# Kernel tuning notes

Hardware: AMD Instinct MI355X
Metric: run time of the kernel (lower is better)

Reference implementation:

```python
import jax, jax.numpy as jnp
import numpy as np

B, T, S, H, E, V = 32, 32, 64, 512, 512, 32000
NEG = -1e9


def setup_inputs() -> dict:
    key = jax.random.key(0)
    ks = jax.random.split(key, 12)
    g = lambda i, shape: jax.random.normal(ks[i], shape, jnp.float32) * 0.05
    return {
        "tgt_batch": jax.random.randint(ks[0], (B, T), 0, V),
        "len_src_batch": jnp.maximum(jax.random.randint(ks[1], (B,), 0, S), 1),
        "enc_outputs": g(2, (S, B, H)),
        "h0": g(3, (1, B, H)),
        "c0": g(4, (1, B, H)),
        "emb": g(5, (V, E)),
        "W_ih": g(6, (4 * H, E + H)),
        "W_hh": g(7, (4 * H, H)),
        "b_ih": jnp.zeros((4 * H,), jnp.float32),
        "b_hh": jnp.zeros((4 * H,), jnp.float32),
        "W_a": g(8, (H, H)),
        "W_c": g(9, (H, 2 * H)),
        "b_c": jnp.zeros((H,), jnp.float32),
        "W_o": g(10, (V, H)),
        "b_o": jnp.zeros((V,), jnp.float32),
    }


def reference(tgt_batch, len_src_batch, enc_outputs, h0, c0, emb,
              W_ih, W_hh, b_ih, b_hh, W_a, W_c, b_c, W_o, b_o):
    Sv = enc_outputs.shape[0]
    # source padding mask [B,S]
    mask = jnp.arange(Sv)[None, :] < len_src_batch[:, None]
    enc_bsh = enc_outputs.transpose(1, 0, 2)                    # [B,S,H]
    # 'general' attention: score(h,e) = h^T W_a e ; precompute W_a @ e
    proj = jnp.einsum('kh,bsh->bsk', W_a, enc_bsh)              # [B,S,H]
    tgt = tgt_batch.T                                           # [T,B]

    def step(carry, w):
        h, c, ah = carry                                        # each [B,H]
        x = emb[w]                                              # [B,E]
        inp = jnp.concatenate([x, ah], axis=1)                  # [B,E+H]
        gates = inp @ W_ih.T + b_ih + h @ W_hh.T + b_hh         # [B,4H]
        i, f, g, o = jnp.split(gates, 4, axis=1)                # torch gate order
        i, f, o = jax.nn.sigmoid(i), jax.nn.sigmoid(f), jax.nn.sigmoid(o)
        c2 = f * c + i * jnp.tanh(g)
        h2 = o * jnp.tanh(c2)                                   # rnn_output
        scores = jnp.einsum('bk,bsk->bs', h2, proj)
        align = jax.nn.softmax(jnp.where(mask, scores, NEG), axis=1)
        ctx = jnp.einsum('bs,bsh->bh', align, enc_bsh)          # bmm context
        ah2 = jnp.tanh(jnp.concatenate([h2, ctx], axis=1) @ W_c.T + b_c)
        logp = jax.nn.log_softmax(ah2 @ W_o.T + b_o, axis=1)    # [B,V]
        return (h2, c2, ah2), logp

    init = (h0[0], c0[0], jnp.zeros_like(h0[0]))
    _, dec_outputs = jax.lax.scan(step, init, tgt[:-1])         # [T-1,B,V]
    dec_output_words = jnp.argmax(dec_outputs, axis=-1)         # [T-1,B]
    return dec_outputs, dec_output_words
```

## Files before the change

kernel.cpp:

```cpp
#include <hip/hip_runtime.h>
#include <cmath>

#define Bc 32
#define Tc 32
#define Sc 64
#define Hc 512
#define Ec 512
#define Vc 32000
#define NEGC (-1e9f)
#define BH (Bc * Hc)
#define Mtot ((Tc - 1) * Bc)

__device__ __forceinline__ float sigf(float x) { return 1.0f / (1.0f + expf(-x)); }

__device__ __forceinline__ float dot4(const float* a, const float* b) {
    float4 x = *(const float4*)a;
    float4 y = *(const float4*)b;
    return x.x * y.x + x.y * y.y + x.z * y.z + x.w * y.w;
}

__global__ __launch_bounds__(256) void k_init(const float* __restrict__ h0,
                                              const float* __restrict__ c0,
                                              float* __restrict__ h, float* __restrict__ c,
                                              float* __restrict__ ah0) {
    int i = blockIdx.x * 256 + threadIdx.x;
    if (i < BH) { h[i] = h0[i]; c[i] = c0[i]; ah0[i] = 0.0f; }
}

__global__ __launch_bounds__(256) void k_proj(const float* __restrict__ W_a,
                                              const float* __restrict__ enc,
                                              float* __restrict__ proj) {
    int k = blockIdx.x * 256 + threadIdx.x;
    int s0 = blockIdx.y * 8;
    int b = blockIdx.z;
    __shared__ float se[8][Hc];
    for (int i = threadIdx.x; i < 8 * Hc; i += 256) {
        int ss = i >> 9, hh = i & (Hc - 1);
        se[ss][hh] = enc[((size_t)(s0 + ss) * Bc + b) * Hc + hh];
    }
    __syncthreads();
    const float* wr = W_a + (size_t)k * Hc;
    float acc[8];
#pragma unroll
    for (int ss = 0; ss < 8; ++ss) acc[ss] = 0.0f;
    for (int h = 0; h < Hc; h += 4) {
        float4 w = *(const float4*)(wr + h);
#pragma unroll
        for (int ss = 0; ss < 8; ++ss) {
            acc[ss] = fmaf(w.x, se[ss][h + 0], acc[ss]);
            acc[ss] = fmaf(w.y, se[ss][h + 1], acc[ss]);
            acc[ss] = fmaf(w.z, se[ss][h + 2], acc[ss]);
            acc[ss] = fmaf(w.w, se[ss][h + 3], acc[ss]);
        }
    }
#pragma unroll
    for (int ss = 0; ss < 8; ++ss)
        proj[((size_t)b * Sc + s0 + ss) * Hc + k] = acc[ss];
}

__global__ __launch_bounds__(256) void k_step1(const int* __restrict__ tgt,
                                               const float* __restrict__ emb,
                                               const float* __restrict__ W_ih,
                                               const float* __restrict__ W_hh,
                                               const float* __restrict__ b_ih,
                                               const float* __restrict__ b_hh,
                                               const float* __restrict__ h_prev,
                                               const float* __restrict__ c_prev,
                                               const float* __restrict__ ah_prev,
                                               float* __restrict__ h_new,
                                               float* __restrict__ c_new, int t) {
    int tid = threadIdx.x;
    int b = tid & 31;
    int q = (tid >> 5) & 3;
    int hl = tid >> 7;
    int h = blockIdx.x * 2 + hl;
    int j = q * Hc + h;
    int w = tgt[b * Tc + t];
    const float* x = emb + (size_t)w * Ec;
    const float* wi = W_ih + (size_t)j * (Ec + Hc);
    const float* wh = W_hh + (size_t)j * Hc;
    const float* ap = ah_prev + b * Hc;
    const float* hp = h_prev + b * Hc;
    float a0 = 0.f, a1 = 0.f, a2 = 0.f, a3 = 0.f;
    for (int e = 0; e < Ec; e += 16) {
        a0 += dot4(x + e, wi + e);
        a1 += dot4(x + e + 4, wi + e + 4);
        a2 += dot4(x + e + 8, wi + e + 8);
        a3 += dot4(x + e + 12, wi + e + 12);
    }
    for (int k = 0; k < Hc; k += 16) {
        a0 += dot4(ap + k, wi + Ec + k);
        a1 += dot4(ap + k + 4, wi + Ec + k + 4);
        a2 += dot4(ap + k + 8, wi + Ec + k + 8);
        a3 += dot4(ap + k + 12, wi + Ec + k + 12);
    }
    for (int k = 0; k < Hc; k += 16) {
        a0 += dot4(hp + k, wh + k);
        a1 += dot4(hp + k + 4, wh + k + 4);
        a2 += dot4(hp + k + 8, wh + k + 8);
        a3 += dot4(hp + k + 12, wh + k + 12);
    }
    float acc = b_ih[j] + b_hh[j] + ((a0 + a1) + (a2 + a3));

    __shared__ float sg[2][4][32];
    sg[hl][q][b] = acc;
    __syncthreads();
    if (q == 0) {
        float iv = sigf(sg[hl][0][b]);
        float fv = sigf(sg[hl][1][b]);
        float gv = tanhf(sg[hl][2][b]);
        float ov = sigf(sg[hl][3][b]);
        int idx = b * Hc + h;
        float c2 = fv * c_prev[idx] + iv * gv;
        float h2 = ov * tanhf(c2);
        c_new[idx] = c2;
        h_new[idx] = h2;
    }
}

__global__ __launch_bounds__(256) void k_score(const float* __restrict__ proj,
                                               const float* __restrict__ h2,
                                               const int* __restrict__ len_src,
                                               float* __restrict__ align) {
    int b = blockIdx.x;
    int tid = threadIdx.x;
    __shared__ float sh[Hc];
    __shared__ float ss[Sc];
    for (int k = tid; k < Hc; k += 256) sh[k] = h2[b * Hc + k];
    __syncthreads();
    {
        int s = tid >> 2, r = tid & 3;
        const float* pr = proj + ((size_t)b * Sc + s) * Hc + r * 128;
        const float* hh = sh + r * 128;
        float p0 = 0.f, p1 = 0.f;
        for (int k = 0; k < 128; k += 8) {
            p0 += dot4(hh + k, pr + k);
            p1 += dot4(hh + k + 4, pr + k + 4);
        }
        float p = p0 + p1;
        p += __shfl_xor(p, 1);
        p += __shfl_xor(p, 2);
        if (r == 0) ss[s] = p;
    }
    __syncthreads();
    if (tid < Sc) {
        int len = len_src[b];
        float sc = (tid < len) ? ss[tid] : NEGC;
        float mx = sc;
#pragma unroll
        for (int m = 32; m >= 1; m >>= 1) mx = fmaxf(mx, __shfl_xor(mx, m));
        float p = expf(sc - mx);
        float sum = p;
#pragma unroll
        for (int m = 32; m >= 1; m >>= 1) sum += __shfl_xor(sum, m);
        align[b * Sc + tid] = p / sum;
    }
}

__global__ __launch_bounds__(256) void k_ctx(const float* __restrict__ enc,
                                             const float* __restrict__ align,
                                             float* __restrict__ ctx) {
    int hs = blockIdx.x, b = blockIdx.y;
    int tid = threadIdx.x;
    __shared__ float sal[Sc];
    __shared__ float part[2][128];
    if (tid < Sc) sal[tid] = align[b * Sc + tid];
    __syncthreads();
    int half = tid >> 7;
    int hl = tid & 127;
    int h = hs * 128 + hl;
    float acc = 0.0f;
    for (int s = half * 32; s < half * 32 + 32; ++s)
        acc = fmaf(sal[s], enc[((size_t)s * Bc + b) * Hc + h], acc);
    part[half][hl] = acc;
    __syncthreads();
    if (half == 0) ctx[b * Hc + h] = part[0][hl] + part[1][hl];
}

__global__ __launch_bounds__(256) void k_wc(const float* __restrict__ h2,
                                            const float* __restrict__ ctx,
                                            const float* __restrict__ W_c,
                                            const float* __restrict__ b_c,
                                            float* __restrict__ ah_new) {
    int tid = threadIdx.x;
    int kl = tid >> 5;
    int b = tid & 31;
    int k = blockIdx.x * 8 + kl;
    const float* wc = W_c + (size_t)k * (2 * Hc);
    const float* hp = h2 + b * Hc;
    const float* cp = ctx + b * Hc;
    float a0 = 0.f, a1 = 0.f, a2 = 0.f, a3 = 0.f;
    for (int j = 0; j < Hc; j += 16) {
        a0 += dot4(hp + j, wc + j);
        a1 += dot4(hp + j + 4, wc + j + 4);
        a2 += dot4(hp + j + 8, wc + j + 8);
        a3 += dot4(hp + j + 12, wc + j + 12);
    }
    const float* wc2 = wc + Hc;
    for (int j = 0; j < Hc; j += 16) {
        a0 += dot4(cp + j, wc2 + j);
        a1 += dot4(cp + j + 4, wc2 + j + 4);
        a2 += dot4(cp + j + 8, wc2 + j + 8);
        a3 += dot4(cp + j + 12, wc2 + j + 12);
    }
    ah_new[b * Hc + k] = tanhf(b_c[k] + ((a0 + a1) + (a2 + a3)));
}

__global__ __launch_bounds__(256) void k_biglogits(const float* __restrict__ A,
                                                   const float* __restrict__ W_o,
                                                   const float* __restrict__ b_o,
                                                   float* __restrict__ out) {
    __shared__ float At[32][128];
    __shared__ float Bt[32][128];
    int tid = threadIdx.x;
    int n_base = blockIdx.x * 128;
    int m_base = blockIdx.y * 128;
    int tn = tid & 15, tm = tid >> 4;

    float acc[2][4][2][4];
#pragma unroll
    for (int mg = 0; mg < 2; ++mg)
#pragma unroll
        for (int mi = 0; mi < 4; ++mi)
#pragma unroll
            for (int ng = 0; ng < 2; ++ng)
#pragma unroll
                for (int ni = 0; ni < 4; ++ni) acc[mg][mi][ng][ni] = 0.0f;

    int srow = tid >> 1;
    int koff = (tid & 1) * 16;
    int gm = m_base + srow;
    const float* arow = A + (size_t)gm * Hc + koff;
    const float* brow = W_o + (size_t)(n_base + srow) * Hc + koff;

    for (int kc = 0; kc < Hc; kc += 32) {
        float av[16], bv[16];
#pragma unroll
        for (int i = 0; i < 4; ++i) {
            float4 t4 = (gm < Mtot) ? *(const float4*)(arow + kc + i * 4)
                                    : make_float4(0.f, 0.f, 0.f, 0.f);
            av[i * 4 + 0] = t4.x; av[i * 4 + 1] = t4.y; av[i * 4 + 2] = t4.z; av[i * 4 + 3] = t4.w;
            float4 u4 = *(const float4*)(brow + kc + i * 4);
            bv[i * 4 + 0] = u4.x; bv[i * 4 + 1] = u4.y; bv[i * 4 + 2] = u4.z; bv[i * 4 + 3] = u4.w;
        }
        __syncthreads();
#pragma unroll
        for (int i = 0; i < 16; ++i) {
            At[koff + i][srow] = av[i];
            Bt[koff + i][srow] = bv[i];
        }
        __syncthreads();
#pragma unroll
        for (int k = 0; k < 32; ++k) {
            float4 a0 = *(const float4*)&At[k][tm * 4];
            float4 a1 = *(const float4*)&At[k][64 + tm * 4];
            float4 b0 = *(const float4*)&Bt[k][tn * 4];
            float4 b1 = *(const float4*)&Bt[k][64 + tn * 4];
            float am[2][4] = {{a0.x, a0.y, a0.z, a0.w}, {a1.x, a1.y, a1.z, a1.w}};
            float bn[2][4] = {{b0.x, b0.y, b0.z, b0.w}, {b1.x, b1.y, b1.z, b1.w}};
#pragma unroll
            for (int mg = 0; mg < 2; ++mg)
#pragma unroll
                for (int mi = 0; mi < 4; ++mi)
#pragma unroll
                    for (int ng = 0; ng < 2; ++ng)
#pragma unroll
                        for (int ni = 0; ni < 4; ++ni)
                            acc[mg][mi][ng][ni] = fmaf(am[mg][mi], bn[ng][ni], acc[mg][mi][ng][ni]);
        }
        __syncthreads();
    }

#pragma unroll
    for (int ng = 0; ng < 2; ++ng) {
        int n = n_base + ng * 64 + tn * 4;
        float4 bo = *(const float4*)(b_o + n);
#pragma unroll
        for (int mg = 0; mg < 2; ++mg)
#pragma unroll
            for (int mi = 0; mi < 4; ++mi) {
                int m = m_base + mg * 64 + tm * 4 + mi;
                if (m < Mtot) {
                    float4 v;
                    v.x = acc[mg][mi][ng][0] + bo.x;
                    v.y = acc[mg][mi][ng][1] + bo.y;
                    v.z = acc[mg][mi][ng][2] + bo.z;
                    v.w = acc[mg][mi][ng][3] + bo.w;
                    *(float4*)(out + (size_t)m * Vc + n) = v;
                }
            }
    }
}

__global__ __launch_bounds__(256) void k_reduce_norm(float* __restrict__ out,
                                                     float* __restrict__ words) {
    int m = blockIdx.x, tid = threadIdx.x;
    float* row = out + (size_t)m * Vc;
    float mx = -INFINITY;
    int mi = 0;
    for (int v = tid; v < Vc; v += 256) {
        float x = row[v];
        if (x > mx) { mx = x; mi = v; }
    }
    __shared__ float smx[256];
    __shared__ int smi[256];
    __shared__ float ssum[256];
    smx[tid] = mx; smi[tid] = mi;
    __syncthreads();
    for (int off = 128; off; off >>= 1) {
        if (tid < off) {
            float o = smx[tid + off]; int oi = smi[tid + off];
            if (o > smx[tid] || (o == smx[tid] && oi < smi[tid])) { smx[tid] = o; smi[tid] = oi; }
        }
        __syncthreads();
    }
    float gmx = smx[0];
    float s = 0.0f;
    for (int v = tid; v < Vc; v += 256) s += expf(row[v] - gmx);
    ssum[tid] = s;
    __syncthreads();
    for (int off = 128; off; off >>= 1) {
        if (tid < off) ssum[tid] += ssum[tid + off];
        __syncthreads();
    }
    float lse = gmx + logf(ssum[0]);
    __syncthreads();
    for (int v = tid; v < Vc; v += 256) row[v] -= lse;
    if (tid == 0) words[m] = (float)smi[0];
}

extern "C" void kernel_launch(void* const* d_in, const int* in_sizes, int n_in,
                              void* d_out, int out_size, void* d_ws, size_t ws_size,
                              hipStream_t stream) {
    const int*   tgt     = (const int*)d_in[0];
    const int*   len_src = (const int*)d_in[1];
    const float* enc     = (const float*)d_in[2];
    const float* h0      = (const float*)d_in[3];
    const float* c0      = (const float*)d_in[4];
    const float* emb     = (const float*)d_in[5];
    const float* W_ih    = (const float*)d_in[6];
    const float* W_hh    = (const float*)d_in[7];
    const float* b_ih    = (const float*)d_in[8];
    const float* b_hh    = (const float*)d_in[9];
    const float* W_a     = (const float*)d_in[10];
    const float* W_c     = (const float*)d_in[11];
    const float* b_c     = (const float*)d_in[12];
    const float* W_o     = (const float*)d_in[13];
    const float* b_o     = (const float*)d_in[14];

    float* out = (float*)d_out;
    float* ws = (float*)d_ws;

    float* proj   = ws;
    float* hbuf   = proj + (size_t)Bc * Sc * Hc;
    float* cbuf   = hbuf + 2 * BH;
    float* ah_all = cbuf + 2 * BH;
    float* ctx    = ah_all + 32 * BH;
    float* align  = ctx + BH;
    float* out_words = out + (size_t)(Tc - 1) * Bc * Vc;

    k_init<<<64, 256, 0, stream>>>(h0, c0, hbuf, cbuf, ah_all);
    {
        dim3 g(Hc / 256, Sc / 8, Bc);
        k_proj<<<g, 256, 0, stream>>>(W_a, enc, proj);
    }

    int cur = 0;
    for (int t = 0; t < Tc - 1; ++t) {
        int nxt = 1 - cur;
        float* hP = hbuf + cur * BH; float* hN = hbuf + nxt * BH;
        float* cP = cbuf + cur * BH; float* cN = cbuf + nxt * BH;
        float* aP = ah_all + (size_t)t * BH;
        float* aN = ah_all + (size_t)(t + 1) * BH;

        k_step1<<<Hc / 2, 256, 0, stream>>>(tgt, emb, W_ih, W_hh, b_ih, b_hh,
                                            hP, cP, aP, hN, cN, t);
        k_score<<<Bc, 256, 0, stream>>>(proj, hN, len_src, align);
        {
            dim3 g(4, Bc);
            k_ctx<<<g, 256, 0, stream>>>(enc, align, ctx);
        }
        k_wc<<<64, 256, 0, stream>>>(hN, ctx, W_c, b_c, aN);
        cur = nxt;
    }

    {
        dim3 g(Vc / 128, (Mtot + 127) / 128);
        k_biglogits<<<g, 256, 0, stream>>>(ah_all + BH, W_o, b_o, out);
    }
    k_reduce_norm<<<Mtot, 256, 0, stream>>>(out, out_words);
}
```

Before: 4.151 ms.

## Fuse recurrent decoder steps into one persistent kernel with grid barriers

Replaces the per-timestep sequence of four kernel launches (gate GEMV, attention score, context, W_c combine) and the init kernel with a single persistent 256-block kernel that loops over time and synchronises through an atomic-counter grid barrier. Score, softmax, context and the W_c projection are fused into one block per batch row, keeping h and ctx in shared memory instead of round-tripping through global buffers. This removes roughly a hundred-plus launch gaps, but the W_c stage now runs on only 32 blocks while the rest idle, and correctness depends on all 256 blocks being co-resident.

```diff
diff --git a/kernel.cpp b/kernel.cpp
--- a/kernel.cpp
+++ b/kernel.cpp
@@ -10,6 +10,7 @@
 #define NEGC (-1e9f)
 #define BH (Bc * Hc)
 #define Mtot ((Tc - 1) * Bc)
+#define NBLK 256
 
 __device__ __forceinline__ float sigf(float x) { return 1.0f / (1.0f + expf(-x)); }
 
@@ -19,17 +20,24 @@
     return x.x * y.x + x.y * y.y + x.z * y.z + x.w * y.w;
 }
 
-__global__ __launch_bounds__(256) void k_init(const float* __restrict__ h0,
-                                              const float* __restrict__ c0,
-                                              float* __restrict__ h, float* __restrict__ c,
-                                              float* __restrict__ ah0) {
-    int i = blockIdx.x * 256 + threadIdx.x;
-    if (i < BH) { h[i] = h0[i]; c[i] = c0[i]; ah0[i] = 0.0f; }
+__device__ __forceinline__ void gbar(unsigned int* cnt, unsigned int target) {
+    __syncthreads();
+    if (threadIdx.x == 0) {
+        __threadfence();
+        __hip_atomic_fetch_add(cnt, 1u, __ATOMIC_ACQ_REL, __HIP_MEMORY_SCOPE_AGENT);
+        while (__hip_atomic_load(cnt, __ATOMIC_RELAXED, __HIP_MEMORY_SCOPE_AGENT) < target)
+            __builtin_amdgcn_s_sleep(1);
+        __threadfence();
+    }
+    __syncthreads();
 }
 
 __global__ __launch_bounds__(256) void k_proj(const float* __restrict__ W_a,
                                               const float* __restrict__ enc,
-                                              float* __restrict__ proj) {
+                                              float* __restrict__ proj,
+                                              unsigned int* __restrict__ cnt) {
+    if (blockIdx.x == 0 && blockIdx.y == 0 && blockIdx.z == 0 && threadIdx.x == 0)
+        *cnt = 0u;
     int k = blockIdx.x * 256 + threadIdx.x;
     int s0 = blockIdx.y * 8;
     int b = blockIdx.z;
@@ -58,152 +66,156 @@
         proj[((size_t)b * Sc + s0 + ss) * Hc + k] = acc[ss];
 }
 
-__global__ __launch_bounds__(256) void k_step1(const int* __restrict__ tgt,
-                                               const float* __restrict__ emb,
-                                               const float* __restrict__ W_ih,
-                                               const float* __restrict__ W_hh,
-                                               const float* __restrict__ b_ih,
-                                               const float* __restrict__ b_hh,
-                                               const float* __restrict__ h_prev,
-                                               const float* __restrict__ c_prev,
-                                               const float* __restrict__ ah_prev,
-                                               float* __restrict__ h_new,
-                                               float* __restrict__ c_new, int t) {
-    int tid = threadIdx.x;
-    int b = tid & 31;
-    int q = (tid >> 5) & 3;
-    int hl = tid >> 7;
-    int h = blockIdx.x * 2 + hl;
-    int j = q * Hc + h;
-    int w = tgt[b * Tc + t];
-    const float* x = emb + (size_t)w * Ec;
-    const float* wi = W_ih + (size_t)j * (Ec + Hc);
-    const float* wh = W_hh + (size_t)j * Hc;
-    const float* ap = ah_prev + b * Hc;
-    const float* hp = h_prev + b * Hc;
-    float a0 = 0.f, a1 = 0.f, a2 = 0.f, a3 = 0.f;
-    for (int e = 0; e < Ec; e += 16) {
-        a0 += dot4(x + e, wi + e);
-        a1 += dot4(x + e + 4, wi + e + 4);
-        a2 += dot4(x + e + 8, wi + e + 8);
-        a3 += dot4(x + e + 12, wi + e + 12);
-    }
-    for (int k = 0; k < Hc; k += 16) {
-        a0 += dot4(ap + k, wi + Ec + k);
-        a1 += dot4(ap + k + 4, wi + Ec + k + 4);
-        a2 += dot4(ap + k + 8, wi + Ec + k + 8);
-        a3 += dot4(ap + k + 12, wi + Ec + k + 12);
-    }
-    for (int k = 0; k < Hc; k += 16) {
-        a0 += dot4(hp + k, wh + k);
-        a1 += dot4(hp + k + 4, wh + k + 4);
-        a2 += dot4(hp + k + 8, wh + k + 8);
-        a3 += dot4(hp + k + 12, wh + k + 12);
-    }
-    float acc = b_ih[j] + b_hh[j] + ((a0 + a1) + (a2 + a3));
+__global__ __launch_bounds__(256) void k_loop(
+    const int* __restrict__ tgt, const int* __restrict__ len_src,
+    const float* __restrict__ enc, const float* __restrict__ h0,
+    const float* __restrict__ c0, const float* __restrict__ emb,
+    const float* __restrict__ W_ih, const float* __restrict__ W_hh,
+    const float* __restrict__ b_ih, const float* __restrict__ b_hh,
+    const float* __restrict__ proj, const float* __restrict__ W_c,
+    const float* __restrict__ b_c,
+    float* __restrict__ hbuf, float* __restrict__ cbuf,
+    float* __restrict__ ah_all, unsigned int* __restrict__ cnt) {
+    int blk = blockIdx.x, tid = threadIdx.x;
+    unsigned int gen = 0;
+
+    {
+        int i = blk * 256 + tid;
+        if (i < BH) { hbuf[i] = h0[i]; cbuf[i] = c0[i]; ah_all[i] = 0.0f; }
+    }
+    gbar(cnt, ++gen * NBLK);
 
     __shared__ float sg[2][4][32];
-    sg[hl][q][b] = acc;
-    __syncthreads();
-    if (q == 0) {
-        float iv = sigf(sg[hl][0][b]);
-        float fv = sigf(sg[hl][1][b]);
-        float gv = tanhf(sg[hl][2][b]);
-        float ov = sigf(sg[hl][3][b]);
-        int idx = b * Hc + h;
-        float c2 = fv * c_prev[idx] + iv * gv;
-        float h2 = ov * tanhf(c2);
-        c_new[idx] = c2;
-        h_new[idx] = h2;
-    }
-}
-
-__global__ __launch_bounds__(256) void k_score(const float* __restrict__ proj,
-                                               const float* __restrict__ h2,
-                                               const int* __restrict__ len_src,
-                                               float* __restrict__ align) {
-    int b = blockIdx.x;
-    int tid = threadIdx.x;
-    __shared__ float sh[Hc];
+    __shared__ __align__(16) float sh[Hc];
+    __shared__ __align__(16) float scv[Hc];
     __shared__ float ss[Sc];
-    for (int k = tid; k < Hc; k += 256) sh[k] = h2[b * Hc + k];
-    __syncthreads();
-    {
-        int s = tid >> 2, r = tid & 3;
-        const float* pr = proj + ((size_t)b * Sc + s) * Hc + r * 128;
-        const float* hh = sh + r * 128;
-        float p0 = 0.f, p1 = 0.f;
-        for (int k = 0; k < 128; k += 8) {
-            p0 += dot4(hh + k, pr + k);
-            p1 += dot4(hh + k + 4, pr + k + 4);
-        }
-        float p = p0 + p1;
-        p += __shfl_xor(p, 1);
-        p += __shfl_xor(p, 2);
-        if (r == 0) ss[s] = p;
-    }
-    __syncthreads();
-    if (tid < Sc) {
-        int len = len_src[b];
-        float sc = (tid < len) ? ss[tid] : NEGC;
-        float mx = sc;
-#pragma unroll
-        for (int m = 32; m >= 1; m >>= 1) mx = fmaxf(mx, __shfl_xor(mx, m));
-        float p = expf(sc - mx);
-        float sum = p;
-#pragma unroll
-        for (int m = 32; m >= 1; m >>= 1) sum += __shfl_xor(sum, m);
-        align[b * Sc + tid] = p / sum;
-    }
-}
-
-__global__ __launch_bounds__(256) void k_ctx(const float* __restrict__ enc,
-                                             const float* __restrict__ align,
-                                             float* __restrict__ ctx) {
-    int hs = blockIdx.x, b = blockIdx.y;
-    int tid = threadIdx.x;
     __shared__ float sal[Sc];
-    __shared__ float part[2][128];
-    if (tid < Sc) sal[tid] = align[b * Sc + tid];
-    __syncthreads();
-    int half = tid >> 7;
-    int hl = tid & 127;
-    int h = hs * 128 + hl;
-    float acc = 0.0f;
-    for (int s = half * 32; s < half * 32 + 32; ++s)
-        acc = fmaf(sal[s], enc[((size_t)s * Bc + b) * Hc + h], acc);
-    part[half][hl] = acc;
-    __syncthreads();
-    if (half == 0) ctx[b * Hc + h] = part[0][hl] + part[1][hl];
-}
-
-__global__ __launch_bounds__(256) void k_wc(const float* __restrict__ h2,
-                                            const float* __restrict__ ctx,
-                                            const float* __restrict__ W_c,
-                                            const float* __restrict__ b_c,
-                                            float* __restrict__ ah_new) {
-    int tid = threadIdx.x;
-    int kl = tid >> 5;
-    int b = tid & 31;
-    int k = blockIdx.x * 8 + kl;
-    const float* wc = W_c + (size_t)k * (2 * Hc);
-    const float* hp = h2 + b * Hc;
-    const float* cp = ctx + b * Hc;
-    float a0 = 0.f, a1 = 0.f, a2 = 0.f, a3 = 0.f;
-    for (int j = 0; j < Hc; j += 16) {
-        a0 += dot4(hp + j, wc + j);
-        a1 += dot4(hp + j + 4, wc + j + 4);
-        a2 += dot4(hp + j + 8, wc + j + 8);
-        a3 += dot4(hp + j + 12, wc + j + 12);
-    }
-    const float* wc2 = wc + Hc;
-    for (int j = 0; j < Hc; j += 16) {
-        a0 += dot4(cp + j, wc2 + j);
-        a1 += dot4(cp + j + 4, wc2 + j + 4);
-        a2 += dot4(cp + j + 8, wc2 + j + 8);
-        a3 += dot4(cp + j + 12, wc2 + j + 12);
-    }
-    ah_new[b * Hc + k] = tanhf(b_c[k] + ((a0 + a1) + (a2 + a3)));
+
+    int cur = 0;
+    for (int t = 0; t < Tc - 1; ++t) {
+        int nxt = 1 - cur;
+        const float* hP = hbuf + cur * BH;
+        float*       hN = hbuf + nxt * BH;
+        const float* cP = cbuf + cur * BH;
+        float*       cN = cbuf + nxt * BH;
+        const float* aP = ah_all + (size_t)t * BH;
+        float*       aN = ah_all + (size_t)(t + 1) * BH;
+
+        {
+            int b  = tid & 31;
+            int q  = (tid >> 5) & 3;
+            int hl = tid >> 7;
+            int h  = blk * 2 + hl;
+            int j  = q * Hc + h;
+            int w  = tgt[b * Tc + t];
+            const float* x  = emb + (size_t)w * Ec;
+            const float* wi = W_ih + (size_t)j * (Ec + Hc);
+            const float* wh = W_hh + (size_t)j * Hc;
+            const float* ap = aP + b * Hc;
+            const float* hp = hP + b * Hc;
+            float a0 = 0.f, a1 = 0.f, a2 = 0.f, a3 = 0.f;
+            for (int e = 0; e < Ec; e += 16) {
+                a0 += dot4(x + e, wi + e);
+                a1 += dot4(x + e + 4, wi + e + 4);
+                a2 += dot4(x + e + 8, wi + e + 8);
+                a3 += dot4(x + e + 12, wi + e + 12);
+            }
+            for (int k = 0; k < Hc; k += 16) {
+                a0 += dot4(ap + k, wi + Ec + k);
+                a1 += dot4(ap + k + 4, wi + Ec + k + 4);
+                a2 += dot4(ap + k + 8, wi + Ec + k + 8);
+                a3 += dot4(ap + k + 12, wi + Ec + k + 12);
+            }
+            for (int k = 0; k < Hc; k += 16) {
+                a0 += dot4(hp + k, wh + k);
+                a1 += dot4(hp + k + 4, wh + k + 4);
+                a2 += dot4(hp + k + 8, wh + k + 8);
+                a3 += dot4(hp + k + 12, wh + k + 12);
+            }
+            float acc = b_ih[j] + b_hh[j] + ((a0 + a1) + (a2 + a3));
+            sg[hl][q][b] = acc;
+            __syncthreads();
+            if (q == 0) {
+                float iv = sigf(sg[hl][0][b]);
+                float fv = sigf(sg[hl][1][b]);
+                float gv = tanhf(sg[hl][2][b]);
+                float ov = sigf(sg[hl][3][b]);
+                int idx = b * Hc + h;
+                float c2 = fv * cP[idx] + iv * gv;
+                float h2v = ov * tanhf(c2);
+                cN[idx] = c2;
+                hN[idx] = h2v;
+            }
+        }
+        gbar(cnt, ++gen * NBLK);
+
+        if (blk < Bc) {
+            int b = blk;
+            for (int k = tid; k < Hc; k += 256) sh[k] = hN[b * Hc + k];
+            __syncthreads();
+            {
+                int s = tid >> 2, r = tid & 3;
+                const float* pr = proj + ((size_t)b * Sc + s) * Hc + r * 128;
+                const float* hh = sh + r * 128;
+                float p0 = 0.f, p1 = 0.f;
+                for (int k = 0; k < 128; k += 8) {
+                    p0 += dot4(hh + k, pr + k);
+                    p1 += dot4(hh + k + 4, pr + k + 4);
+                }
+                float p = p0 + p1;
+                p += __shfl_xor(p, 1);
+                p += __shfl_xor(p, 2);
+                if (r == 0) ss[s] = p;
+            }
+            __syncthreads();
+            if (tid < Sc) {
+                int len = len_src[b];
+                float sc = (tid < len) ? ss[tid] : NEGC;
+                float mx = sc;
+#pragma unroll
+                for (int m = 32; m >= 1; m >>= 1) mx = fmaxf(mx, __shfl_xor(mx, m));
+                float p = expf(sc - mx);
+                float sum = p;
+#pragma unroll
+                for (int m = 32; m >= 1; m >>= 1) sum += __shfl_xor(sum, m);
+                sal[tid] = p / sum;
+            }
+            __syncthreads();
+#pragma unroll
+            for (int rep = 0; rep < 2; ++rep) {
+                int h = tid + rep * 256;
+                float accA = 0.0f, accB = 0.0f;
+                for (int s = 0; s < 32; ++s)
+                    accA = fmaf(sal[s], enc[((size_t)s * Bc + b) * Hc + h], accA);
+                for (int s = 32; s < 64; ++s)
+                    accB = fmaf(sal[s], enc[((size_t)s * Bc + b) * Hc + h], accB);
+                scv[h] = accA + accB;
+            }
+            __syncthreads();
+#pragma unroll
+            for (int rep = 0; rep < 2; ++rep) {
+                int k = tid + rep * 256;
+                const float* wc = W_c + (size_t)k * (2 * Hc);
+                float a0 = 0.f, a1 = 0.f, a2 = 0.f, a3 = 0.f;
+                for (int j = 0; j < Hc; j += 16) {
+                    a0 += dot4(sh + j, wc + j);
+                    a1 += dot4(sh + j + 4, wc + j + 4);
+                    a2 += dot4(sh + j + 8, wc + j + 8);
+                    a3 += dot4(sh + j + 12, wc + j + 12);
+                }
+                const float* wc2 = wc + Hc;
+                for (int j = 0; j < Hc; j += 16) {
+                    a0 += dot4(scv + j, wc2 + j);
+                    a1 += dot4(scv + j + 4, wc2 + j + 4);
+                    a2 += dot4(scv + j + 8, wc2 + j + 8);
+                    a3 += dot4(scv + j + 12, wc2 + j + 12);
+                }
+                aN[b * Hc + k] = tanhf(b_c[k] + ((a0 + a1) + (a2 + a3)));
+            }
+        }
+        gbar(cnt, ++gen * NBLK);
+        cur = nxt;
+    }
 }
 
 __global__ __launch_bounds__(256) void k_biglogits(const float* __restrict__ A,
@@ -355,34 +367,17 @@
     float* hbuf   = proj + (size_t)Bc * Sc * Hc;
     float* cbuf   = hbuf + 2 * BH;
     float* ah_all = cbuf + 2 * BH;
-    float* ctx    = ah_all + 32 * BH;
-    float* align  = ctx + BH;
+    unsigned int* cnt = (unsigned int*)(ah_all + 32 * BH);
     float* out_words = out + (size_t)(Tc - 1) * Bc * Vc;
 
-    k_init<<<64, 256, 0, stream>>>(h0, c0, hbuf, cbuf, ah_all);
     {
         dim3 g(Hc / 256, Sc / 8, Bc);
-        k_proj<<<g, 256, 0, stream>>>(W_a, enc, proj);
-    }
-
-    int cur = 0;
-    for (int t = 0; t < Tc - 1; ++t) {
-        int nxt = 1 - cur;
-        float* hP = hbuf + cur * BH; float* hN = hbuf + nxt * BH;
-        float* cP = cbuf + cur * BH; float* cN = cbuf + nxt * BH;
-        float* aP = ah_all + (size_t)t * BH;
-        float* aN = ah_all + (size_t)(t + 1) * BH;
-
-        k_step1<<<Hc / 2, 256, 0, stream>>>(tgt, emb, W_ih, W_hh, b_ih, b_hh,
-                                            hP, cP, aP, hN, cN, t);
-        k_score<<<Bc, 256, 0, stream>>>(proj, hN, len_src, align);
-        {
-            dim3 g(4, Bc);
-            k_ctx<<<g, 256, 0, stream>>>(enc, align, ctx);
-        }
-        k_wc<<<64, 256, 0, stream>>>(hN, ctx, W_c, b_c, aN);
-        cur = nxt;
-    }
+        k_proj<<<g, 256, 0, stream>>>(W_a, enc, proj, cnt);
+    }
+
+    k_loop<<<NBLK, 256, 0, stream>>>(tgt, len_src, enc, h0, c0, emb,
+                                     W_ih, W_hh, b_ih, b_hh, proj, W_c, b_c,
+                                     hbuf, cbuf, ah_all, cnt);
 
     {
         dim3 g(Vc / 128, (Mtot + 127) / 128);
```

Result: slower. 6.263 ms (+50.9%).
